# Kernel optimization log

Hardware: AMD Instinct MI355X
Metric: run time of the kernel (lower is better)

Reference implementation:

```python
import jax, jax.numpy as jnp
import numpy as np

EMBED_DIM = 1024
NUM_HEADS = 16
HEAD_DIM = EMBED_DIM // NUM_HEADS


def setup_inputs() -> dict:
    key = jax.random.key(0)
    ks = jax.random.split(key, 9)
    B, S, D = 2, 2048, EMBED_DIM
    scale = 1.0 / np.sqrt(D)
    inp = {
        "x": jax.random.normal(ks[0], (B, S, D), dtype=jnp.float32),
        "w_q": jax.random.normal(ks[1], (D, D), dtype=jnp.float32) * scale,
        "b_q": jnp.zeros((D,), dtype=jnp.float32),
        "w_k": jax.random.normal(ks[2], (D, D), dtype=jnp.float32) * scale,
        "b_k": jnp.zeros((D,), dtype=jnp.float32),
        "w_v": jax.random.normal(ks[3], (D, D), dtype=jnp.float32) * scale,
        "b_v": jnp.zeros((D,), dtype=jnp.float32),
        "w_o": jax.random.normal(ks[4], (D, D), dtype=jnp.float32) * scale,
        "b_o": jnp.zeros((D,), dtype=jnp.float32),
    }
    return inp


def reference(x, w_q, b_q, w_k, b_k, w_v, b_v, w_o, b_o):
    B, S, D = x.shape
    H, Hd = NUM_HEADS, HEAD_DIM

    def proj(w, b):
        # (B,S,D) @ (D,D) -> (B,S,D) -> (B,H,S,Hd)
        y = jnp.einsum('bsd,df->bsf', x, w) + b
        return y.reshape(B, S, H, Hd).transpose(0, 2, 1, 3)

    q = proj(w_q, b_q)
    k = proj(w_k, b_k)
    v = proj(w_v, b_v)

    scores = jnp.einsum('bhqd,bhkd->bhqk', q, k) / jnp.sqrt(jnp.float32(Hd))
    attn = jax.nn.softmax(scores, axis=-1)
    context = jnp.einsum('bhqk,bhkd->bhqd', attn, v)
    context = context.transpose(0, 2, 1, 3).reshape(B, S, D)
    return jnp.einsum('bsd,df->bsf', context + x, w_o) + b_o
```

## Files before the change

### kernel.cpp

```cpp
#include <hip/hip_runtime.h>
#include <hip/hip_bf16.h>

typedef _Float16 f16;
typedef _Float16 f16x8 __attribute__((ext_vector_type(8)));
typedef _Float16 f16x4 __attribute__((ext_vector_type(4)));
typedef float f32x4 __attribute__((ext_vector_type(4)));

#define EMBED 1024
#define NHEAD 16
#define HDIM 64
#define SEQ 2048
#define BATCH 2
#define NROW (BATCH * SEQ)
#define PSTR 72
#define WBYTES (2 * 64 * PSTR * 2)
#define MBIAS 14.4269504089f
#define QSCALE 0.1803368801f

__device__ __forceinline__ void gld_lds16(const f16* g, f16* l) {
    __builtin_amdgcn_global_load_lds(
        (const __attribute__((address_space(1))) void*)g,
        (__attribute__((address_space(3))) void*)l, 16, 0, 0);
}

__global__ void k_prep(const float* __restrict__ wq, const float* __restrict__ wk,
                       const float* __restrict__ wv, const float* __restrict__ wo,
                       const float* __restrict__ x,
                       f16* __restrict__ wqkvt, f16* __restrict__ wot, f16* __restrict__ xb) {
    if (blockIdx.z >= 4) {
        int i = (((blockIdx.z - 4) * 1024 + blockIdx.y * 32 + blockIdx.x) * 256 + threadIdx.x) * 4;
        float4 v = *(const float4*)&x[i];
        f16x4 o = {(f16)v.x, (f16)v.y, (f16)v.z, (f16)v.w};
        *(f16x4*)&xb[i] = o;
        return;
    }
    const float* W;
    f16* Wt;
    switch (blockIdx.z) {
        case 0: W = wq; Wt = wqkvt; break;
        case 1: W = wk; Wt = wqkvt + 1024 * 1024; break;
        case 2: W = wv; Wt = wqkvt + 2 * 1024 * 1024; break;
        default: W = wo; Wt = wot; break;
    }
    __shared__ float t[32][33];
    int tx = threadIdx.x & 31, ty = threadIdx.x >> 5;
    int r0 = blockIdx.y * 32, c0 = blockIdx.x * 32;
    for (int j = 0; j < 4; ++j)
        t[ty + j * 8][tx] = W[(r0 + ty + j * 8) * 1024 + c0 + tx];
    __syncthreads();
    for (int j = 0; j < 4; ++j)
        Wt[(c0 + ty + j * 8) * 1024 + r0 + tx] = (f16)t[tx][ty + j * 8];
}

__global__ void k_bias(const float* __restrict__ bq, const float* __restrict__ bk,
                       const float* __restrict__ bv, float* __restrict__ bias) {
    int i = blockIdx.x * blockDim.x + threadIdx.x;
    if (i < 3072) bias[i] = (i < 1024) ? bq[i] : ((i < 2048) ? bk[i - 1024] : bv[i - 2048]);
}

template <bool SWAP>
__device__ __forceinline__ void gemm_kloop(const f16* __restrict__ A, const f16* __restrict__ Bt,
                                           int K, f16* Al, f16* Bl, int m0, int n0,
                                           int w, int quad, int l16, int mw, int nw,
                                           int crow, int ccol, f32x4 (&acc)[4][4]) {
    for (int k0 = 0; k0 < K; k0 += 32) {
        __syncthreads();
        gld_lds16(&A[(m0 + crow) * K + k0 + ccol], &Al[(w * 64) * 8]);
        gld_lds16(&A[(m0 + 64 + crow) * K + k0 + ccol], &Al[(256 + w * 64) * 8]);
        gld_lds16(&Bt[(n0 + crow) * K + k0 + ccol], &Bl[(w * 64) * 8]);
        gld_lds16(&Bt[(n0 + 64 + crow) * K + k0 + ccol], &Bl[(256 + w * 64) * 8]);
        __syncthreads();
        f16x8 af[4], bf[4];
        for (int i = 0; i < 4; ++i)
            af[i] = *(const f16x8*)&Al[(mw + i * 16 + l16) * 32 + quad * 8];
        for (int j = 0; j < 4; ++j)
            bf[j] = *(const f16x8*)&Bl[(nw + j * 16 + l16) * 32 + quad * 8];
        for (int i = 0; i < 4; ++i)
            for (int j = 0; j < 4; ++j)
                acc[i][j] = SWAP
                    ? __builtin_amdgcn_mfma_f32_16x16x32_f16(bf[j], af[i], acc[i][j], 0, 0, 0)
                    : __builtin_amdgcn_mfma_f32_16x16x32_f16(af[i], bf[j], acc[i][j], 0, 0, 0);
    }
}

__global__ __launch_bounds__(256) void k_gemm_qkv(const f16* __restrict__ A, const f16* __restrict__ Bt,
                                                  const float* __restrict__ bias,
                                                  f16* __restrict__ qk, f16* __restrict__ Vt) {
    __shared__ __align__(16) f16 Al[128 * 32];
    __shared__ __align__(16) f16 Bl[128 * 32];
    const int K = 1024;
    int tid = threadIdx.x;
    int w = tid >> 6, lane = tid & 63, quad = lane >> 4, l16 = lane & 15;
    int m0 = blockIdx.x * 128, n0 = blockIdx.y * 128;
    int mw = (w >> 1) * 64, nw = (w & 1) * 64;
    int c = w * 64 + lane;
    int crow = c >> 2, ccol = (c & 3) * 8;
    f32x4 acc[4][4] = {};

    if (n0 >= 2048) {
        gemm_kloop<true>(A, Bt, K, Al, Bl, m0, n0, w, quad, l16, mw, nw, crow, ccol, acc);
        for (int i = 0; i < 4; ++i) {
            int mrow = m0 + mw + i * 16 + l16;
            int b = mrow >> 11, s = mrow & 2047;
            for (int j = 0; j < 4; ++j)
                for (int r = 0; r < 4; ++r) {
                    int col = n0 + nw + j * 16 + quad * 4 + r;
                    int d = col - 2048;
                    Vt[(b * 1024 + d) * SEQ + s] = (f16)(acc[i][j][r] + bias[col]);
                }
        }
    } else {
        gemm_kloop<false>(A, Bt, K, Al, Bl, m0, n0, w, quad, l16, mw, nw, crow, ccol, acc);
        for (int i = 0; i < 4; ++i) {
            int row = m0 + mw + i * 16 + quad * 4;
            for (int j = 0; j < 4; ++j) {
                int col = n0 + nw + j * 16 + l16;
                float bval = bias[col];
                for (int r = 0; r < 4; ++r)
                    qk[(row + r) * 2048 + col] = (f16)(acc[i][j][r] + bval);
            }
        }
    }
}

__global__ __launch_bounds__(256) void k_gemm_out(const f16* __restrict__ A, const f16* __restrict__ Bt,
                                                  const float* __restrict__ bias, float* __restrict__ Cout) {
    __shared__ __align__(16) f16 Al[128 * 32];
    __shared__ __align__(16) f16 Bl[64 * 32];
    const int K = 1024, N = 1024;
    int tid = threadIdx.x;
    int w = tid >> 6, lane = tid & 63, quad = lane >> 4, l16 = lane & 15;
    int m0 = blockIdx.x * 128, n0 = blockIdx.y * 64;
    int mw = (w >> 1) * 64, nw = (w & 1) * 32;
    int c = w * 64 + lane;
    int crow = c >> 2, ccol = (c & 3) * 8;
    f32x4 acc[4][2] = {};

    for (int k0 = 0; k0 < K; k0 += 32) {
        __syncthreads();
        gld_lds16(&A[(m0 + crow) * K + k0 + ccol], &Al[(w * 64) * 8]);
        gld_lds16(&A[(m0 + 64 + crow) * K + k0 + ccol], &Al[(256 + w * 64) * 8]);
        gld_lds16(&Bt[(n0 + crow) * K + k0 + ccol], &Bl[(w * 64) * 8]);
        __syncthreads();
        f16x8 af[4], bf[2];
        for (int i = 0; i < 4; ++i)
            af[i] = *(const f16x8*)&Al[(mw + i * 16 + l16) * 32 + quad * 8];
        for (int j = 0; j < 2; ++j)
            bf[j] = *(const f16x8*)&Bl[(nw + j * 16 + l16) * 32 + quad * 8];
        for (int i = 0; i < 4; ++i)
            for (int j = 0; j < 2; ++j)
                acc[i][j] = __builtin_amdgcn_mfma_f32_16x16x32_f16(af[i], bf[j], acc[i][j], 0, 0, 0);
    }

    for (int i = 0; i < 4; ++i) {
        int row = m0 + mw + i * 16 + quad * 4;
        for (int j = 0; j < 2; ++j) {
            int col = n0 + nw + j * 16 + l16;
            float bval = bias[col];
            for (int r = 0; r < 4; ++r)
                Cout[(row + r) * N + col] = acc[i][j][r] + bval;
        }
    }
}

__global__ __launch_bounds__(256, 2) void k_attn(const f16* __restrict__ qk, const f16* __restrict__ Vt,
                                                 const float* __restrict__ x, f16* __restrict__ ctx) {
    __shared__ __align__(16) char smem[4 * WBYTES];

    int tid = threadIdx.x;
    int w = tid >> 6, lane = tid & 63, quad = lane >> 4, l16 = lane & 15;
    int q0 = blockIdx.x * 64;
    int bh = blockIdx.y, b = bh >> 4, h = bh & 15;
    int kbase = 1024 + h * 64;
    int qcol = h * 64;
    int vbase = b * 1024 + h * 64;

    f16* Kw = (f16*)(smem + w * WBYTES);
    f16* Vw = Kw + 64 * PSTR;
    f16* Pw = Kw;

    f16x8 qf[4][2];
    for (int qg = 0; qg < 4; ++qg) {
        int qrow = b * SEQ + q0 + qg * 16 + l16;
        for (int kk = 0; kk < 2; ++kk) {
            f16x8 v = *(const f16x8*)&qk[qrow * 2048 + qcol + kk * 32 + quad * 8];
            for (int e = 0; e < 8; ++e) v[e] = (f16)((float)v[e] * QSCALE);
            qf[qg][kk] = v;
        }
    }

    int srow = lane >> 3;
    int scol = (lane & 7) * 8;
    const f16* kgp = &qk[(b * SEQ + w * 512 + srow) * 2048 + kbase + scol];
    const f16* vgp = &Vt[(vbase + srow) * SEQ + w * 512 + scol];

    f32x4 oacc[4][4] = {};
    float li[4] = {0.f, 0.f, 0.f, 0.f};

    for (int kt = 0; kt < 8; ++kt) {
        f16x8 tk[8], tv[8];
        for (int c = 0; c < 8; ++c) {
            tk[c] = *(const f16x8*)(kgp + c * 8 * 2048);
            tv[c] = *(const f16x8*)(vgp + c * 8 * SEQ);
        }
        kgp += 64 * 2048;
        vgp += 64;
        for (int c = 0; c < 8; ++c) {
            *(f16x8*)&Kw[(c * 8 + srow) * PSTR + scol] = tk[c];
            *(f16x8*)&Vw[(c * 8 + srow) * PSTR + scol] = tv[c];
        }

        f16x8 kf[4][2];
        for (int nt = 0; nt < 4; ++nt)
            for (int kk = 0; kk < 2; ++kk)
                kf[nt][kk] = *(const f16x8*)&Kw[(nt * 16 + l16) * PSTR + kk * 32 + quad * 8];
        asm volatile("s_waitcnt lgkmcnt(0)" ::: "memory");

        for (int qg = 0; qg < 4; ++qg) {
            f32x4 st[4];
            for (int nt = 0; nt < 4; ++nt) {
                f32x4 s = {};
                s = __builtin_amdgcn_mfma_f32_16x16x32_f16(kf[nt][0], qf[qg][0], s, 0, 0, 0);
                s = __builtin_amdgcn_mfma_f32_16x16x32_f16(kf[nt][1], qf[qg][1], s, 0, 0, 0);
                st[nt] = s;
            }
            float rs = 0.f;
            for (int nt = 0; nt < 4; ++nt)
                for (int r = 0; r < 4; ++r) {
                    float p = __builtin_amdgcn_exp2f(st[nt][r] - MBIAS);
                    st[nt][r] = p;
                    rs += p;
                }
            rs += __shfl_xor(rs, 16);
            rs += __shfl_xor(rs, 32);
            li[qg] += rs;
            for (int nt = 0; nt < 4; ++nt) {
                f16x4 pk;
                for (int r = 0; r < 4; ++r) pk[r] = (f16)st[nt][r];
                *(f16x4*)&Pw[(qg * 16 + l16) * PSTR + nt * 16 + quad * 4] = pk;
            }
        }
        asm volatile("s_waitcnt lgkmcnt(0)" ::: "memory");

        f16x8 pf[4][2];
        for (int qg = 0; qg < 4; ++qg)
            for (int kk = 0; kk < 2; ++kk)
                pf[qg][kk] = *(const f16x8*)&Pw[(qg * 16 + l16) * PSTR + kk * 32 + quad * 8];
        for (int nt = 0; nt < 4; ++nt) {
            f16x8 vf0 = *(const f16x8*)&Vw[(nt * 16 + l16) * PSTR + quad * 8];
            f16x8 vf1 = *(const f16x8*)&Vw[(nt * 16 + l16) * PSTR + 32 + quad * 8];
            for (int qg = 0; qg < 4; ++qg) {
                oacc[qg][nt] = __builtin_amdgcn_mfma_f32_16x16x32_f16(pf[qg][0], vf0, oacc[qg][nt], 0, 0, 0);
                oacc[qg][nt] = __builtin_amdgcn_mfma_f32_16x16x32_f16(pf[qg][1], vf1, oacc[qg][nt], 0, 0, 0);
            }
        }
    }

    __syncthreads();
    float* Ow = (float*)(smem + w * WBYTES);
    float* Lw = (float*)(smem + w * WBYTES + 16384);
    for (int qg = 0; qg < 4; ++qg)
        for (int nt = 0; nt < 4; ++nt)
            for (int r = 0; r < 4; ++r)
                Ow[(qg * 16 + quad * 4 + r) * 64 + nt * 16 + l16] = oacc[qg][nt][r];
    if (quad == 0)
        for (int qg = 0; qg < 4; ++qg) Lw[qg * 16 + l16] = li[qg];
    __syncthreads();

    int q = tid >> 2, d0 = (tid & 3) * 16;
    f32x4 a4[4] = {};
    float lsum = 0.f;
    for (int w2 = 0; w2 < 4; ++w2) {
        const float* Ow2 = (const float*)(smem + w2 * WBYTES);
        const float* Lw2 = (const float*)(smem + w2 * WBYTES + 16384);
        for (int j = 0; j < 4; ++j)
            a4[j] += *(const f32x4*)&Ow2[q * 64 + d0 + 4 * j];
        lsum += Lw2[q];
    }
    int g = b * SEQ + q0 + q;
    int cb = h * 64 + d0;
    float inv = 1.f / lsum;
    f16x8 o0, o1;
    for (int j = 0; j < 4; ++j) {
        float4 xv = *(const float4*)&x[g * 1024 + cb + 4 * j];
        float4 r;
        r.x = a4[j][0] * inv + xv.x;
        r.y = a4[j][1] * inv + xv.y;
        r.z = a4[j][2] * inv + xv.z;
        r.w = a4[j][3] * inv + xv.w;
        f16* dst = (j < 2) ? (f16*)&o0 : (f16*)&o1;
        int o = (j & 1) * 4;
        dst[o + 0] = (f16)r.x; dst[o + 1] = (f16)r.y; dst[o + 2] = (f16)r.z; dst[o + 3] = (f16)r.w;
    }
    *(f16x8*)&ctx[g * 1024 + cb] = o0;
    *(f16x8*)&ctx[g * 1024 + cb + 8] = o1;
}

extern "C" void kernel_launch(void* const* d_in, const int* in_sizes, int n_in,
                              void* d_out, int out_size, void* d_ws, size_t ws_size,
                              hipStream_t stream) {
    const float* x  = (const float*)d_in[0];
    const float* wq = (const float*)d_in[1];
    const float* bq = (const float*)d_in[2];
    const float* wk = (const float*)d_in[3];
    const float* bk = (const float*)d_in[4];
    const float* wv = (const float*)d_in[5];
    const float* bv = (const float*)d_in[6];
    const float* wo = (const float*)d_in[7];
    const float* bo = (const float*)d_in[8];
    float* out = (float*)d_out;

    char* ws = (char*)d_ws;
    f16*   xb    = (f16*)(ws);
    f16*   wqkvt = (f16*)(ws + (8u << 20));
    f16*   wot   = (f16*)(ws + (14u << 20));
    float* biasq = (float*)(ws + (16u << 20));
    f16*   qkbuf = (f16*)(ws + (16u << 20) + (64u << 10));
    f16*   vtbuf = (f16*)(ws + (32u << 20) + (64u << 10));
    f16*   ctx   = xb;

    k_prep<<<dim3(32, 32, 8), 256, 0, stream>>>(wq, wk, wv, wo, x, wqkvt, wot, xb);
    k_bias<<<12, 256, 0, stream>>>(bq, bk, bv, biasq);

    k_gemm_qkv<<<dim3(32, 24), 256, 0, stream>>>(xb, wqkvt, biasq, qkbuf, vtbuf);
    k_attn<<<dim3(SEQ / 64, BATCH * NHEAD), 256, 0, stream>>>(qkbuf, vtbuf, x, ctx);
    k_gemm_out<<<dim3(32, 16), 256, 0, stream>>>(ctx, wot, bo, out);
}
```

Measured before the change: 216.8 us.

## Store Q/K/V in MFMA fragment order so attention loads fragments directly from global

The QKV GEMM epilogue now writes Q, K and V into a pre-swizzled fragment layout matching the attention kernel's MFMA operand order. Attention can then load K and V fragments straight from global memory instead of staging them through LDS, and the SWAP template flag is flipped between the V and Q/K paths. LDS drops to just the P buffer, which permits raising launch bounds to 3 blocks per CU, and the cross-wave output reduction is done per 16-row group with a padded stride. The trade-off is scattered 8-byte epilogue stores, more global load traffic per wave (no LDS reuse), and extra syncthreads in the reduction.

```diff
diff --git a/kernel.cpp b/kernel.cpp
--- a/kernel.cpp
+++ b/kernel.cpp
@@ -13,7 +13,8 @@
 #define BATCH 2
 #define NROW (BATCH * SEQ)
 #define PSTR 72
-#define WBYTES (2 * 64 * PSTR * 2)
+#define PWB (64 * PSTR * 2)
+#define OSTR 65
 #define MBIAS 14.4269504089f
 #define QSCALE 0.1803368801f
 
@@ -85,7 +86,8 @@
 
 __global__ __launch_bounds__(256) void k_gemm_qkv(const f16* __restrict__ A, const f16* __restrict__ Bt,
                                                   const float* __restrict__ bias,
-                                                  f16* __restrict__ qk, f16* __restrict__ Vt) {
+                                                  f16* __restrict__ Qf, f16* __restrict__ Kf,
+                                                  f16* __restrict__ Vf) {
     __shared__ __align__(16) f16 Al[128 * 32];
     __shared__ __align__(16) f16 Bl[128 * 32];
     const int K = 1024;
@@ -98,26 +100,44 @@
     f32x4 acc[4][4] = {};
 
     if (n0 >= 2048) {
-        gemm_kloop<true>(A, Bt, K, Al, Bl, m0, n0, w, quad, l16, mw, nw, crow, ccol, acc);
-        for (int i = 0; i < 4; ++i) {
-            int mrow = m0 + mw + i * 16 + l16;
-            int b = mrow >> 11, s = mrow & 2047;
-            for (int j = 0; j < 4; ++j)
-                for (int r = 0; r < 4; ++r) {
-                    int col = n0 + nw + j * 16 + quad * 4 + r;
-                    int d = col - 2048;
-                    Vt[(b * 1024 + d) * SEQ + s] = (f16)(acc[i][j][r] + bias[col]);
-                }
-        }
-    } else {
         gemm_kloop<false>(A, Bt, K, Al, Bl, m0, n0, w, quad, l16, mw, nw, crow, ccol, acc);
         for (int i = 0; i < 4; ++i) {
-            int row = m0 + mw + i * 16 + quad * 4;
+            int tok0 = m0 + mw + i * 16 + quad * 4;
+            int b = tok0 >> 11;
+            int tk = (tok0 & 2047) >> 6;
+            int key0 = tok0 & 63;
+            int kk = key0 >> 5, quadf = (key0 >> 3) & 3, j0 = key0 & 7;
             for (int j = 0; j < 4; ++j) {
-                int col = n0 + nw + j * 16 + l16;
-                float bval = bias[col];
-                for (int r = 0; r < 4; ++r)
-                    qk[(row + r) * 2048 + col] = (f16)(acc[i][j][r] + bval);
+                int cd = n0 + nw + j * 16 + l16 - 2048;
+                int h = cd >> 6, d = cd & 63, nt = d >> 4;
+                float bv = bias[2048 + cd];
+                int base = ((((b * 16 + h) * 32 + tk) * 8 + nt * 2 + kk) * 64 + quadf * 16 + (d & 15)) * 8 + j0;
+                f16x4 pk;
+                for (int r = 0; r < 4; ++r) pk[r] = (f16)(acc[i][j][r] + bv);
+                *(f16x4*)&Vf[base] = pk;
+            }
+        }
+    } else {
+        gemm_kloop<true>(A, Bt, K, Al, Bl, m0, n0, w, quad, l16, mw, nw, crow, ccol, acc);
+        f16* dst = (n0 < 1024) ? Qf : Kf;
+        for (int i = 0; i < 4; ++i) {
+            int tokf = m0 + mw + i * 16 + l16;
+            int b = tokf >> 11;
+            int tok = tokf & 2047;
+            int tile = tok >> 6, ntq = (tok >> 4) & 3, l16f = tok & 15;
+            for (int j = 0; j < 4; ++j) {
+                int c0 = n0 + nw + j * 16 + quad * 4;
+                int h = (c0 >> 6) & 15;
+                int d0 = c0 & 63;
+                int kk = d0 >> 5, quadf = (d0 >> 3) & 3, j0 = d0 & 7;
+                float4 bv = *(const float4*)&bias[c0];
+                int base = ((((b * 16 + h) * 32 + tile) * 8 + ntq * 2 + kk) * 64 + quadf * 16 + l16f) * 8 + j0;
+                f16x4 pk;
+                pk[0] = (f16)(acc[i][j][0] + bv.x);
+                pk[1] = (f16)(acc[i][j][1] + bv.y);
+                pk[2] = (f16)(acc[i][j][2] + bv.z);
+                pk[3] = (f16)(acc[i][j][3] + bv.w);
+                *(f16x4*)&dst[base] = pk;
             }
         }
     }
@@ -163,58 +183,40 @@
     }
 }
 
-__global__ __launch_bounds__(256, 2) void k_attn(const f16* __restrict__ qk, const f16* __restrict__ Vt,
-                                                 const float* __restrict__ x, f16* __restrict__ ctx) {
-    __shared__ __align__(16) char smem[4 * WBYTES];
+__global__ __launch_bounds__(256, 3) void k_attn(const f16* __restrict__ Qf, const f16* __restrict__ Kf,
+                                                 const f16* __restrict__ Vf, const float* __restrict__ x,
+                                                 f16* __restrict__ ctx) {
+    __shared__ __align__(16) char smem[4 * PWB + 1024];
 
     int tid = threadIdx.x;
     int w = tid >> 6, lane = tid & 63, quad = lane >> 4, l16 = lane & 15;
-    int q0 = blockIdx.x * 64;
+    int qtile = blockIdx.x, q0 = qtile * 64;
     int bh = blockIdx.y, b = bh >> 4, h = bh & 15;
-    int kbase = 1024 + h * 64;
-    int qcol = h * 64;
-    int vbase = b * 1024 + h * 64;
-
-    f16* Kw = (f16*)(smem + w * WBYTES);
-    f16* Vw = Kw + 64 * PSTR;
-    f16* Pw = Kw;
-
+
+    f16* Pw = (f16*)(smem + w * PWB);
+    float* Li = (float*)(smem + 4 * PWB);
+
+    const f16* qp = Qf + (bh * 32 + qtile) * 4096 + lane * 8;
     f16x8 qf[4][2];
-    for (int qg = 0; qg < 4; ++qg) {
-        int qrow = b * SEQ + q0 + qg * 16 + l16;
+    for (int qg = 0; qg < 4; ++qg)
         for (int kk = 0; kk < 2; ++kk) {
-            f16x8 v = *(const f16x8*)&qk[qrow * 2048 + qcol + kk * 32 + quad * 8];
+            f16x8 v = *(const f16x8*)(qp + (qg * 2 + kk) * 512);
             for (int e = 0; e < 8; ++e) v[e] = (f16)((float)v[e] * QSCALE);
             qf[qg][kk] = v;
         }
-    }
-
-    int srow = lane >> 3;
-    int scol = (lane & 7) * 8;
-    const f16* kgp = &qk[(b * SEQ + w * 512 + srow) * 2048 + kbase + scol];
-    const f16* vgp = &Vt[(vbase + srow) * SEQ + w * 512 + scol];
+
+    const f16* kp = Kf + (bh * 32 + w * 8) * 4096 + lane * 8;
+    const f16* vp = Vf + (bh * 32 + w * 8) * 4096 + lane * 8;
 
     f32x4 oacc[4][4] = {};
     float li[4] = {0.f, 0.f, 0.f, 0.f};
 
     for (int kt = 0; kt < 8; ++kt) {
-        f16x8 tk[8], tv[8];
-        for (int c = 0; c < 8; ++c) {
-            tk[c] = *(const f16x8*)(kgp + c * 8 * 2048);
-            tv[c] = *(const f16x8*)(vgp + c * 8 * SEQ);
-        }
-        kgp += 64 * 2048;
-        vgp += 64;
-        for (int c = 0; c < 8; ++c) {
-            *(f16x8*)&Kw[(c * 8 + srow) * PSTR + scol] = tk[c];
-            *(f16x8*)&Vw[(c * 8 + srow) * PSTR + scol] = tv[c];
-        }
-
         f16x8 kf[4][2];
         for (int nt = 0; nt < 4; ++nt)
             for (int kk = 0; kk < 2; ++kk)
-                kf[nt][kk] = *(const f16x8*)&Kw[(nt * 16 + l16) * PSTR + kk * 32 + quad * 8];
-        asm volatile("s_waitcnt lgkmcnt(0)" ::: "memory");
+                kf[nt][kk] = *(const f16x8*)(kp + (nt * 2 + kk) * 512);
+        kp += 4096;
 
         for (int qg = 0; qg < 4; ++qg) {
             f32x4 st[4];
@@ -247,53 +249,47 @@
             for (int kk = 0; kk < 2; ++kk)
                 pf[qg][kk] = *(const f16x8*)&Pw[(qg * 16 + l16) * PSTR + kk * 32 + quad * 8];
         for (int nt = 0; nt < 4; ++nt) {
-            f16x8 vf0 = *(const f16x8*)&Vw[(nt * 16 + l16) * PSTR + quad * 8];
-            f16x8 vf1 = *(const f16x8*)&Vw[(nt * 16 + l16) * PSTR + 32 + quad * 8];
+            f16x8 vf0 = *(const f16x8*)(vp + (nt * 2 + 0) * 512);
+            f16x8 vf1 = *(const f16x8*)(vp + (nt * 2 + 1) * 512);
             for (int qg = 0; qg < 4; ++qg) {
                 oacc[qg][nt] = __builtin_amdgcn_mfma_f32_16x16x32_f16(pf[qg][0], vf0, oacc[qg][nt], 0, 0, 0);
                 oacc[qg][nt] = __builtin_amdgcn_mfma_f32_16x16x32_f16(pf[qg][1], vf1, oacc[qg][nt], 0, 0, 0);
             }
         }
-    }
-
+        vp += 4096;
+    }
+
+    if (quad == 0)
+        for (int qg = 0; qg < 4; ++qg) Li[w * 64 + qg * 16 + l16] = li[qg];
     __syncthreads();
-    float* Ow = (float*)(smem + w * WBYTES);
-    float* Lw = (float*)(smem + w * WBYTES + 16384);
-    for (int qg = 0; qg < 4; ++qg)
+
+    float* Ow = (float*)(smem + w * PWB);
+    int q16 = tid >> 4;
+    int d0 = (tid & 15) * 4;
+    for (int qg = 0; qg < 4; ++qg) {
         for (int nt = 0; nt < 4; ++nt)
             for (int r = 0; r < 4; ++r)
-                Ow[(qg * 16 + quad * 4 + r) * 64 + nt * 16 + l16] = oacc[qg][nt][r];
-    if (quad == 0)
-        for (int qg = 0; qg < 4; ++qg) Lw[qg * 16 + l16] = li[qg];
-    __syncthreads();
-
-    int q = tid >> 2, d0 = (tid & 3) * 16;
-    f32x4 a4[4] = {};
-    float lsum = 0.f;
-    for (int w2 = 0; w2 < 4; ++w2) {
-        const float* Ow2 = (const float*)(smem + w2 * WBYTES);
-        const float* Lw2 = (const float*)(smem + w2 * WBYTES + 16384);
-        for (int j = 0; j < 4; ++j)
-            a4[j] += *(const f32x4*)&Ow2[q * 64 + d0 + 4 * j];
-        lsum += Lw2[q];
-    }
-    int g = b * SEQ + q0 + q;
-    int cb = h * 64 + d0;
-    float inv = 1.f / lsum;
-    f16x8 o0, o1;
-    for (int j = 0; j < 4; ++j) {
-        float4 xv = *(const float4*)&x[g * 1024 + cb + 4 * j];
-        float4 r;
-        r.x = a4[j][0] * inv + xv.x;
-        r.y = a4[j][1] * inv + xv.y;
-        r.z = a4[j][2] * inv + xv.z;
-        r.w = a4[j][3] * inv + xv.w;
-        f16* dst = (j < 2) ? (f16*)&o0 : (f16*)&o1;
-        int o = (j & 1) * 4;
-        dst[o + 0] = (f16)r.x; dst[o + 1] = (f16)r.y; dst[o + 2] = (f16)r.z; dst[o + 3] = (f16)r.w;
-    }
-    *(f16x8*)&ctx[g * 1024 + cb] = o0;
-    *(f16x8*)&ctx[g * 1024 + cb + 8] = o1;
+                Ow[(quad * 4 + r) * OSTR + nt * 16 + l16] = oacc[qg][nt][r];
+        __syncthreads();
+        f32x4 a = {};
+        float lsum = 0.f;
+        for (int w2 = 0; w2 < 4; ++w2) {
+            const float* Ow2 = (const float*)(smem + w2 * PWB);
+            a += *(const f32x4*)&Ow2[q16 * OSTR + d0];
+            lsum += Li[w2 * 64 + qg * 16 + q16];
+        }
+        int g = b * SEQ + q0 + qg * 16 + q16;
+        int cb = h * 64 + d0;
+        float inv = 1.f / lsum;
+        float4 xv = *(const float4*)&x[g * 1024 + cb];
+        f16x4 o;
+        o[0] = (f16)(a[0] * inv + xv.x);
+        o[1] = (f16)(a[1] * inv + xv.y);
+        o[2] = (f16)(a[2] * inv + xv.z);
+        o[3] = (f16)(a[3] * inv + xv.w);
+        *(f16x4*)&ctx[g * 1024 + cb] = o;
+        __syncthreads();
+    }
 }
 
 extern "C" void kernel_launch(void* const* d_in, const int* in_sizes, int n_in,
@@ -315,14 +311,15 @@
     f16*   wqkvt = (f16*)(ws + (8u << 20));
     f16*   wot   = (f16*)(ws + (14u << 20));
     float* biasq = (float*)(ws + (16u << 20));
-    f16*   qkbuf = (f16*)(ws + (16u << 20) + (64u << 10));
-    f16*   vtbuf = (f16*)(ws + (32u << 20) + (64u << 10));
+    f16*   Qfb   = (f16*)(ws + (16u << 20) + (64u << 10));
+    f16*   Kfb   = (f16*)(ws + (24u << 20) + (64u << 10));
+    f16*   Vfb   = (f16*)(ws + (32u << 20) + (64u << 10));
     f16*   ctx   = xb;
 
     k_prep<<<dim3(32, 32, 8), 256, 0, stream>>>(wq, wk, wv, wo, x, wqkvt, wot, xb);
     k_bias<<<12, 256, 0, stream>>>(bq, bk, bv, biasq);
 
-    k_gemm_qkv<<<dim3(32, 24), 256, 0, stream>>>(xb, wqkvt, biasq, qkbuf, vtbuf);
-    k_attn<<<dim3(SEQ / 64, BATCH * NHEAD), 256, 0, stream>>>(qkbuf, vtbuf, x, ctx);
+    k_gemm_qkv<<<dim3(32, 24), 256, 0, stream>>>(xb, wqkvt, biasq, Qfb, Kfb, Vfb);
+    k_attn<<<dim3(SEQ / 64, BATCH * NHEAD), 256, 0, stream>>>(Qfb, Kfb, Vfb, x, ctx);
     k_gemm_out<<<dim3(32, 16), 256, 0, stream>>>(ctx, wot, bo, out);
 }
```

After: 250.8 us. +15.7%, slower.

## Load K/V MFMA fragments directly from global and raise attention occupancy

Applied to the files above, without the earlier changes.

The attention kernel stops staging K and V tiles through shared memory. Each lane now reads its MFMA operand fragments straight from global memory, so shared memory holds only the per-wave P buffer and the row-sum array. This roughly halves the shared-memory footprint, and the launch bound rises from 2 to 4 blocks per SM to hide load latency with more resident waves. The epilogue now reduces the partial outputs one 16-row group at a time through a padded fp32 buffer, at the cost of extra barriers and possible misaligned 16-byte LDS reads from the odd stride.

```diff
diff --git a/kernel.cpp b/kernel.cpp
--- a/kernel.cpp
+++ b/kernel.cpp
@@ -13,7 +13,8 @@
 #define BATCH 2
 #define NROW (BATCH * SEQ)
 #define PSTR 72
-#define WBYTES (2 * 64 * PSTR * 2)
+#define PWB (64 * PSTR * 2)
+#define OSTR 65
 #define MBIAS 14.4269504089f
 #define QSCALE 0.1803368801f
 
@@ -163,9 +164,9 @@
     }
 }
 
-__global__ __launch_bounds__(256, 2) void k_attn(const f16* __restrict__ qk, const f16* __restrict__ Vt,
+__global__ __launch_bounds__(256, 4) void k_attn(const f16* __restrict__ qk, const f16* __restrict__ Vt,
                                                  const float* __restrict__ x, f16* __restrict__ ctx) {
-    __shared__ __align__(16) char smem[4 * WBYTES];
+    __shared__ __align__(16) char smem[4 * PWB + 1024];
 
     int tid = threadIdx.x;
     int w = tid >> 6, lane = tid & 63, quad = lane >> 4, l16 = lane & 15;
@@ -175,9 +176,8 @@
     int qcol = h * 64;
     int vbase = b * 1024 + h * 64;
 
-    f16* Kw = (f16*)(smem + w * WBYTES);
-    f16* Vw = Kw + 64 * PSTR;
-    f16* Pw = Kw;
+    f16* Pw = (f16*)(smem + w * PWB);
+    float* Li = (float*)(smem + 4 * PWB);
 
     f16x8 qf[4][2];
     for (int qg = 0; qg < 4; ++qg) {
@@ -189,32 +189,18 @@
         }
     }
 
-    int srow = lane >> 3;
-    int scol = (lane & 7) * 8;
-    const f16* kgp = &qk[(b * SEQ + w * 512 + srow) * 2048 + kbase + scol];
-    const f16* vgp = &Vt[(vbase + srow) * SEQ + w * 512 + scol];
+    const f16* kp = &qk[(b * SEQ + w * 512 + l16) * 2048 + kbase + quad * 8];
+    const f16* vp = &Vt[(vbase + l16) * SEQ + w * 512 + quad * 8];
 
     f32x4 oacc[4][4] = {};
     float li[4] = {0.f, 0.f, 0.f, 0.f};
 
     for (int kt = 0; kt < 8; ++kt) {
-        f16x8 tk[8], tv[8];
-        for (int c = 0; c < 8; ++c) {
-            tk[c] = *(const f16x8*)(kgp + c * 8 * 2048);
-            tv[c] = *(const f16x8*)(vgp + c * 8 * SEQ);
-        }
-        kgp += 64 * 2048;
-        vgp += 64;
-        for (int c = 0; c < 8; ++c) {
-            *(f16x8*)&Kw[(c * 8 + srow) * PSTR + scol] = tk[c];
-            *(f16x8*)&Vw[(c * 8 + srow) * PSTR + scol] = tv[c];
-        }
-
         f16x8 kf[4][2];
         for (int nt = 0; nt < 4; ++nt)
             for (int kk = 0; kk < 2; ++kk)
-                kf[nt][kk] = *(const f16x8*)&Kw[(nt * 16 + l16) * PSTR + kk * 32 + quad * 8];
-        asm volatile("s_waitcnt lgkmcnt(0)" ::: "memory");
+                kf[nt][kk] = *(const f16x8*)(kp + nt * 16 * 2048 + kk * 32);
+        kp += 64 * 2048;
 
         for (int qg = 0; qg < 4; ++qg) {
             f32x4 st[4];
@@ -247,53 +233,47 @@
             for (int kk = 0; kk < 2; ++kk)
                 pf[qg][kk] = *(const f16x8*)&Pw[(qg * 16 + l16) * PSTR + kk * 32 + quad * 8];
         for (int nt = 0; nt < 4; ++nt) {
-            f16x8 vf0 = *(const f16x8*)&Vw[(nt * 16 + l16) * PSTR + quad * 8];
-            f16x8 vf1 = *(const f16x8*)&Vw[(nt * 16 + l16) * PSTR + 32 + quad * 8];
+            f16x8 vf0 = *(const f16x8*)(vp + nt * 16 * SEQ);
+            f16x8 vf1 = *(const f16x8*)(vp + nt * 16 * SEQ + 32);
             for (int qg = 0; qg < 4; ++qg) {
                 oacc[qg][nt] = __builtin_amdgcn_mfma_f32_16x16x32_f16(pf[qg][0], vf0, oacc[qg][nt], 0, 0, 0);
                 oacc[qg][nt] = __builtin_amdgcn_mfma_f32_16x16x32_f16(pf[qg][1], vf1, oacc[qg][nt], 0, 0, 0);
             }
         }
-    }
-
+        vp += 64;
+    }
+
+    if (quad == 0)
+        for (int qg = 0; qg < 4; ++qg) Li[w * 64 + qg * 16 + l16] = li[qg];
     __syncthreads();
-    float* Ow = (float*)(smem + w * WBYTES);
-    float* Lw = (float*)(smem + w * WBYTES + 16384);
-    for (int qg = 0; qg < 4; ++qg)
+
+    float* Ow = (float*)(smem + w * PWB);
+    int q16 = tid >> 4;
+    int d0 = (tid & 15) * 4;
+    for (int qg = 0; qg < 4; ++qg) {
         for (int nt = 0; nt < 4; ++nt)
             for (int r = 0; r < 4; ++r)
-                Ow[(qg * 16 + quad * 4 + r) * 64 + nt * 16 + l16] = oacc[qg][nt][r];
-    if (quad == 0)
-        for (int qg = 0; qg < 4; ++qg) Lw[qg * 16 + l16] = li[qg];
-    __syncthreads();
-
-    int q = tid >> 2, d0 = (tid & 3) * 16;
-    f32x4 a4[4] = {};
-    float lsum = 0.f;
-    for (int w2 = 0; w2 < 4; ++w2) {
-        const float* Ow2 = (const float*)(smem + w2 * WBYTES);
-        const float* Lw2 = (const float*)(smem + w2 * WBYTES + 16384);
-        for (int j = 0; j < 4; ++j)
-            a4[j] += *(const f32x4*)&Ow2[q * 64 + d0 + 4 * j];
-        lsum += Lw2[q];
-    }
-    int g = b * SEQ + q0 + q;
-    int cb = h * 64 + d0;
-    float inv = 1.f / lsum;
-    f16x8 o0, o1;
-    for (int j = 0; j < 4; ++j) {
-        float4 xv = *(const float4*)&x[g * 1024 + cb + 4 * j];
-        float4 r;
-        r.x = a4[j][0] * inv + xv.x;
-        r.y = a4[j][1] * inv + xv.y;
-        r.z = a4[j][2] * inv + xv.z;
-        r.w = a4[j][3] * inv + xv.w;
-        f16* dst = (j < 2) ? (f16*)&o0 : (f16*)&o1;
-        int o = (j & 1) * 4;
-        dst[o + 0] = (f16)r.x; dst[o + 1] = (f16)r.y; dst[o + 2] = (f16)r.z; dst[o + 3] = (f16)r.w;
-    }
-    *(f16x8*)&ctx[g * 1024 + cb] = o0;
-    *(f16x8*)&ctx[g * 1024 + cb + 8] = o1;
+                Ow[(quad * 4 + r) * OSTR + nt * 16 + l16] = oacc[qg][nt][r];
+        __syncthreads();
+        f32x4 a = {};
+        float lsum = 0.f;
+        for (int w2 = 0; w2 < 4; ++w2) {
+            const float* Ow2 = (const float*)(smem + w2 * PWB);
+            a += *(const f32x4*)&Ow2[q16 * OSTR + d0];
+            lsum += Li[w2 * 64 + qg * 16 + q16];
+        }
+        int g = b * SEQ + q0 + qg * 16 + q16;
+        int cb = h * 64 + d0;
+        float inv = 1.f / lsum;
+        float4 xv = *(const float4*)&x[g * 1024 + cb];
+        f16x4 o;
+        o[0] = (f16)(a[0] * inv + xv.x);
+        o[1] = (f16)(a[1] * inv + xv.y);
+        o[2] = (f16)(a[2] * inv + xv.z);
+        o[3] = (f16)(a[3] * inv + xv.w);
+        *(f16x4*)&ctx[g * 1024 + cb] = o;
+        __syncthreads();
+    }
 }
 
 extern "C" void kernel_launch(void* const* d_in, const int* in_sizes, int n_in,
```

After: 342.5 us. +58.0%, slower.
